# Kernel optimization log

Measured on AMD Instinct MI355X. Metric: run time of the kernel, lower is better.

## Reference

```python
import jax, jax.numpy as jnp
import numpy as np

B, N, E, D, H, HW, L = 16, 32, 256, 256, 8, 784, 4
DH = D // H
FF = 4 * D
BN = B * N
BE = B * E
SCALE = 1.0 / np.sqrt(DH)


def _ln(x, g, b):
    m = x.mean(-1, keepdims=True)
    v = ((x - m) ** 2).mean(-1, keepdims=True)
    return (x - m) * jax.lax.rsqrt(v + 1e-5) * g + b


def setup_inputs() -> dict:
    key = jax.random.key(0)
    ks = iter(jax.random.split(key, 64))
    def w(shape, s=0.05):
        return jax.random.normal(next(ks), shape, jnp.float32) * s
    inp = {
        'nodes': w((B, N, D), 1.0),
        'edges': w((B, E, D), 1.0),
        'images': w((B, HW, D), 1.0),
        'mask': jnp.zeros((B * H, N + E, HW), jnp.float32),
        'node_enc': w((BN, D), 1.0),
        'edge_enc': w((BE, D), 1.0),
        'ln1_g': jnp.ones((L, D), jnp.float32), 'ln1_b': jnp.zeros((L, D), jnp.float32),
        'Wqkv': w((L, D, 3 * D)), 'bqkv': jnp.zeros((L, 3 * D), jnp.float32),
        'Wo': w((L, D, D)), 'bo': jnp.zeros((L, D), jnp.float32),
        'ls1': jnp.full((L, D), 0.1, jnp.float32),
        'ln2_g': jnp.ones((L, D), jnp.float32), 'ln2_b': jnp.zeros((L, D), jnp.float32),
        'Wn1': w((L, D, D)), 'bn1': jnp.zeros((L, D), jnp.float32),
        'Wn2': w((L, D, D)), 'bn2': jnp.zeros((L, D), jnp.float32),
        'We': w((L, D, D)), 'be': jnp.zeros((L, D), jnp.float32),
        'attn_p': w((L, H, DH), 1.0),
        'Weo': w((L, D, D)), 'beo': jnp.zeros((L, D), jnp.float32),
        'Wno': w((L, D, D)), 'bno': jnp.zeros((L, D), jnp.float32),
        'ls2': jnp.full((L, D), 0.1, jnp.float32),
        'ln3_g': jnp.ones((L, D), jnp.float32), 'ln3_b': jnp.zeros((L, D), jnp.float32),
        'W1': w((L, D, FF)), 'b1': jnp.zeros((L, FF), jnp.float32),
        'W2': w((L, FF, D)), 'b2': jnp.zeros((L, D), jnp.float32),
        'ls3': jnp.full((L, D), 0.1, jnp.float32),
        'edge_index': jax.random.randint(next(ks), (2, BE), 0, BN, jnp.int32),
    }
    return inp


def reference(nodes, edges, images, mask, node_enc, edge_enc,
              ln1_g, ln1_b, Wqkv, bqkv, Wo, bo, ls1,
              ln2_g, ln2_b, Wn1, bn1, Wn2, bn2, We, be, attn_p, Weo, beo, Wno, bno, ls2,
              ln3_g, ln3_b, W1, b1, W2, b2, ls3, edge_index):
    idx0, idx1 = edge_index[0], edge_index[1]
    ne = jnp.concatenate([nodes, edges], axis=1)  # [B, N+E, D]
    mask4 = mask.reshape(B, H, N + E, HW)
    for l in range(L):
        # cross-attention ne -> images
        ne1n = _ln(ne, ln1_g[l], ln1_b[l])
        q = (ne1n @ Wqkv[l, :, :D] + bqkv[l, :D]).reshape(B, N + E, H, DH)
        k = (images @ Wqkv[l, :, D:2 * D] + bqkv[l, D:2 * D]).reshape(B, HW, H, DH)
        v = (images @ Wqkv[l, :, 2 * D:] + bqkv[l, 2 * D:]).reshape(B, HW, H, DH)
        scores = jnp.einsum('bqhd,bkhd->bhqk', q, k) * SCALE + mask4
        attn = jax.nn.softmax(scores, axis=-1)
        ctx = jnp.einsum('bhqk,bkhd->bqhd', attn, v).reshape(B, N + E, D)
        ne1 = ne + ls1[l] * (ctx @ Wo[l] + bo[l])
        # modified GAT on flattened graph
        ne2n = _ln(ne1, ln2_g[l], ln2_b[l])
        nodes_f = ne2n[:, :N].reshape(BN, D) + node_enc
        edges_f = ne2n[:, N:].reshape(BE, D) + edge_enc
        fn = (nodes_f @ Wn1[l] + bn1[l])[idx0]
        sn = (nodes_f @ Wn2[l] + bn2[l])[idx0]  # NOTE: original code uses edge_index[0] here too
        ep = edges_f @ We[l] + be[l]
        hidden = jax.nn.gelu(fn + sn + ep, approximate=False)  # [BE, D]
        pres = (hidden.reshape(BE, H, DH) * attn_p[l]).sum(-1)  # [BE, H]
        mseg = jax.ops.segment_max(pres, idx0, num_segments=BN)
        expv = jnp.exp(pres - mseg[idx0])
        denom = jax.ops.segment_sum(expv, idx0, num_segments=BN)
        alpha = expv / denom[idx0]  # scatter_softmax over destination nodes
        new_edges = hidden @ Weo[l] + beo[l]
        vals = (nodes_f[idx1] + new_edges) @ Wno[l] + bno[l]
        vals = vals.reshape(BE, H, DH) * alpha[..., None]
        new_nodes = jax.ops.segment_sum(vals.reshape(BE, D), idx0, num_segments=BN)
        gat = jnp.concatenate([new_nodes.reshape(B, N, D), new_edges.reshape(B, E, D)], axis=1)
        ne2 = ne1 + ls2[l] * gat
        # FFN
        ne3n = _ln(ne2, ln3_g[l], ln3_b[l])
        ffn = jax.nn.gelu(ne3n @ W1[l] + b1[l], approximate=False) @ W2[l] + b2[l]
        ne = ne2 + ls3[l] * ffn
    return ne
```

## Files before the change

kernel.cpp:

```cpp
#include <hip/hip_runtime.h>
#include <math.h>

static constexpr int B_  = 16;
static constexpr int N_  = 32;
static constexpr int E_  = 256;
static constexpr int D_  = 256;
static constexpr int H_  = 8;
static constexpr int HW_ = 784;
static constexpr int L_  = 4;
static constexpr int DH_ = 32;
static constexpr int FF_ = 1024;
static constexpr int BN_ = 512;
static constexpr int BE_ = 4096;
static constexpr int NE_ = 288;
static constexpr int NC_ = 13;
static constexpr int NBLK_ = B_ * H_ * 9;
#define SCALE_ 0.17677669529663687f

static constexpr size_t LAYER_W = 1114112;
static constexpr size_t OFF_Q   = 0;
static constexpr size_t OFF_K   = 65536;
static constexpr size_t OFF_WO  = 196608;
static constexpr size_t OFF_WN1 = 262144;
static constexpr size_t OFF_WE  = 393216;
static constexpr size_t OFF_WEO = 458752;
static constexpr size_t OFF_WNO = 524288;
static constexpr size_t OFF_W1  = 589824;
static constexpr size_t OFF_W2  = 851968;

typedef __attribute__((ext_vector_type(8))) short bf16x8;
typedef __attribute__((ext_vector_type(4))) float f32x4;

typedef __attribute__((address_space(1))) const unsigned int gas_uint;
typedef __attribute__((address_space(3))) unsigned int las_uint;

__device__ __forceinline__ void gload16(const unsigned short* g, unsigned short* lds) {
    __builtin_amdgcn_global_load_lds((gas_uint*)g, (las_uint*)lds, 16, 0, 0);
}

__device__ __forceinline__ float gelu_f(float x) {
    return 0.5f * x * (1.0f + erff(x * 0.7071067811865476f));
}

__device__ __forceinline__ unsigned short f2bf(float x) {
    unsigned u = __float_as_uint(x);
    u += 0x7FFFu + ((u >> 16) & 1u);
    return (unsigned short)(u >> 16);
}
__device__ __forceinline__ unsigned pack2bf(float a, float b) {
    return (unsigned)f2bf(a) | ((unsigned)f2bf(b) << 16);
}
__device__ __forceinline__ float bf2f(unsigned short u) {
    return __uint_as_float(((unsigned)u) << 16);
}


__global__ void concat_kernel(const float* __restrict__ nodes, const float* __restrict__ edges,
                              float* __restrict__ ne) {
    int tid = blockIdx.x * 256 + threadIdx.x;
    int d = tid & 255;
    int row = tid >> 8;
    int b = row / NE_, pos = row % NE_;
    float v = (pos < N_) ? nodes[(size_t)(b * N_ + pos) * D_ + d]
                         : edges[(size_t)(b * E_ + (pos - N_)) * D_ + d];
    ne[tid] = v;
}

__global__ void imgcast_kernel(const float* __restrict__ img, unsigned short* __restrict__ out) {
    int tid = blockIdx.x * 256 + threadIdx.x;
    const float* p = img + (size_t)tid * 8;
    float4 a = *(const float4*)(p);
    float4 b = *(const float4*)(p + 4);
    uint4 o = make_uint4(pack2bf(a.x, a.y), pack2bf(a.z, a.w),
                         pack2bf(b.x, b.y), pack2bf(b.z, b.w));
    *(uint4*)&out[(size_t)tid * 8] = o;
}

__global__ __launch_bounds__(128) void premask_kernel(const float* __restrict__ mask,
                                                      unsigned short* __restrict__ pmask) {
    const int bid = blockIdx.x;
    const int c = bid % NC_;
    const int bq = bid / NC_;
    const int h = bq & 7;
    const int qt = (bq >> 3) % 9;
    const int b = (bq >> 3) / 9;
    const int q0 = qt * 32, c0 = c * 64;
    __shared__ float ts[32][68];
    const int t = threadIdx.x;
    const int row = t >> 2, cg = (t & 3) * 16;
    const float* mrow = mask + ((size_t)(b * H_ + h) * NE_ + q0 + row) * (size_t)HW_;
    #pragma unroll
    for (int i = 0; i < 4; ++i) {
        int col = c0 + cg + i * 4;
        float4 m4;
        if (col + 4 <= HW_) {
            m4 = *(const float4*)(mrow + col);
        } else {
            m4.x = (col + 0 < HW_) ? mrow[col + 0] : -1e30f;
            m4.y = (col + 1 < HW_) ? mrow[col + 1] : -1e30f;
            m4.z = (col + 2 < HW_) ? mrow[col + 2] : -1e30f;
            m4.w = (col + 3 < HW_) ? mrow[col + 3] : -1e30f;
        }
        *(float4*)&ts[row][cg + i * 4] = m4;
    }
    __syncthreads();
    const int w = t >> 6, lg = (t & 63) >> 4, lr = t & 15;
    const int r0 = w * 16 + lg * 4;
    unsigned u[8];
    #pragma unroll
    for (int rg = 0; rg < 4; ++rg) {
        u[rg * 2 + 0] = pack2bf(ts[r0 + rg][0 * 16 + lr], ts[r0 + rg][1 * 16 + lr]);
        u[rg * 2 + 1] = pack2bf(ts[r0 + rg][2 * 16 + lr], ts[r0 + rg][3 * 16 + lr]);
    }
    uint4* dst = (uint4*)(pmask + (size_t)bid * 2048 + t * 16);
    dst[0] = make_uint4(u[0], u[1], u[2], u[3]);
    dst[1] = make_uint4(u[4], u[5], u[6], u[7]);
}

__device__ __forceinline__ float ln_from_val(float v, int d,
                                             const float* __restrict__ g, const float* __restrict__ bta,
                                             float* sh1, float* sh2) {
    float s = v, s2 = v * v;
    #pragma unroll
    for (int o = 32; o >= 1; o >>= 1) { s += __shfl_down(s, o); s2 += __shfl_down(s2, o); }
    int lane = d & 63, w = d >> 6;
    if (lane == 0) { sh1[w] = s; sh2[w] = s2; }
    __syncthreads();
    if (d == 0) {
        float a = sh1[0] + sh1[1] + sh1[2] + sh1[3];
        float c = sh2[0] + sh2[1] + sh2[2] + sh2[3];
        sh1[0] = a; sh2[0] = c;
    }
    __syncthreads();
    float mean = sh1[0] * (1.0f / D_);
    float var  = sh2[0] * (1.0f / D_) - mean * mean;
    float rstd = rsqrtf(var + 1e-5f);
    return (v - mean) * rstd * g[d] + bta[d];
}

__global__ __launch_bounds__(256) void ln_kernel(const float* __restrict__ x,
                                                 unsigned short* __restrict__ y,
                                                 const float* __restrict__ g,
                                                 const float* __restrict__ bta) {
    __shared__ float sh1[4], sh2[4];
    const int row = blockIdx.x, d = threadIdx.x;
    float v = x[(size_t)row * D_ + d];
    y[(size_t)row * D_ + d] = f2bf(ln_from_val(v, d, g, bta, sh1, sh2));
}

__global__ __launch_bounds__(256) void ln2enc_kernel(const float* __restrict__ x,
                                                     const float* __restrict__ g,
                                                     const float* __restrict__ bta,
                                                     const float* __restrict__ node_enc,
                                                     const float* __restrict__ edge_enc,
                                                     unsigned short* __restrict__ nodes_f,
                                                     unsigned short* __restrict__ edges_f) {
    __shared__ float sh1[4], sh2[4];
    const int row = blockIdx.x, d = threadIdx.x;
    float v = x[(size_t)row * D_ + d];
    float val = ln_from_val(v, d, g, bta, sh1, sh2);
    int b = row / NE_, pos = row % NE_;
    if (pos < N_) {
        int rn = b * N_ + pos;
        nodes_f[(size_t)rn * D_ + d] = f2bf(val + node_enc[(size_t)rn * D_ + d]);
    } else {
        int re = b * E_ + (pos - N_);
        edges_f[(size_t)re * D_ + d] = f2bf(val + edge_enc[(size_t)re * D_ + d]);
    }
}

__global__ __launch_bounds__(256) void gatres_ln_kernel(
    float* __restrict__ ne, const float* __restrict__ new_nodes,
    const float* __restrict__ new_edges, const float* __restrict__ ls2l,
    const float* __restrict__ g, const float* __restrict__ bta,
    unsigned short* __restrict__ lnb) {
    __shared__ float sh1[4], sh2[4];
    const int row = blockIdx.x, d = threadIdx.x;
    int b = row / NE_, pos = row % NE_;
    float gv = (pos < N_) ? new_nodes[(size_t)(b * N_ + pos) * D_ + d]
                          : new_edges[(size_t)(b * E_ + (pos - N_)) * D_ + d];
    float v = ne[(size_t)row * D_ + d] + ls2l[d] * gv;
    ne[(size_t)row * D_ + d] = v;
    lnb[(size_t)row * D_ + d] = f2bf(ln_from_val(v, d, g, bta, sh1, sh2));
}

__global__ __launch_bounds__(256) void wtrans_kernel(
    const float* __restrict__ Wqkv, const float* __restrict__ Wo,
    const float* __restrict__ Wn1,  const float* __restrict__ Wn2,
    const float* __restrict__ We,   const float* __restrict__ Weo,
    const float* __restrict__ Wno,  const float* __restrict__ W1,
    const float* __restrict__ W2,   unsigned short* __restrict__ wT)
{
    const int bid = blockIdx.x;
    const int l = bid / 1088;
    int tl = bid % 1088;
    const float* src; int ld, K, Nn; unsigned short* dst;
    if (tl < 576) {
        int mid = tl >> 6; tl &= 63;
        K = 256; Nn = 256;
        if (mid < 3) {
            src = Wqkv + (size_t)l * 256 * 768 + mid * 256; ld = 768;
            dst = wT + (size_t)l * LAYER_W + (size_t)mid * 65536;
        } else {
            const float* bases[6] = {Wo, Wn1, Wn2, We, Weo, Wno};
            src = bases[mid - 3] + (size_t)l * 65536; ld = 256;
            dst = wT + (size_t)l * LAYER_W + OFF_WO + (size_t)(mid - 3) * 65536;
        }
    } else if (tl < 832) {
        tl -= 576; K = 256; Nn = 1024;
        src = W1 + (size_t)l * 262144; ld = 1024;
        dst = wT + (size_t)l * LAYER_W + OFF_W1;
    } else {
        tl -= 832; K = 1024; Nn = 256;
        src = W2 + (size_t)l * 262144; ld = 256;
        dst = wT + (size_t)l * LAYER_W + OFF_W2;
    }
    const int ntn = Nn >> 5;
    const int k0 = (tl / ntn) << 5, n0 = (tl % ntn) << 5;
    __shared__ float ts[32][33];
    const int t = threadIdx.x;
    const int kl = t >> 5, nl = t & 31;
    #pragma unroll
    for (int rr = 0; rr < 4; ++rr)
        ts[kl + rr * 8][nl] = src[(size_t)(k0 + kl + rr * 8) * ld + n0 + nl];
    __syncthreads();
    const int onl = t >> 3, okl = (t & 7) << 2;
    ushort4 o;
    o.x = f2bf(ts[okl + 0][onl]); o.y = f2bf(ts[okl + 1][onl]);
    o.z = f2bf(ts[okl + 2][onl]); o.w = f2bf(ts[okl + 3][onl]);
    *(ushort4*)&dst[(size_t)(n0 + onl) * K + k0 + okl] = o;
}

template<int MODE, int OUTBF>
__global__ __launch_bounds__(256) void mgemm_kernel(
    const unsigned short* __restrict__ A, int lda,
    const unsigned short* __restrict__ Bt,
    const float* __restrict__ bias,
    const float* __restrict__ bias2,
    const float* __restrict__ res,
    const float* __restrict__ ls,
    void* __restrict__ Cv, int ldc, int K)
{
    __shared__ __align__(16) unsigned short As[64 * 64];
    __shared__ __align__(16) unsigned short Bs[64 * 64];
    const int m0 = blockIdx.y * 64, n0 = blockIdx.x * 64;
    const int t = threadIdx.x;
    const int l = t & 63, w = t >> 6;
    const int wr = (w >> 1) * 32, wc = (w & 1) * 32;
    const int frow = l & 15, kg = l >> 4;
    const int srow = w * 8 + (l >> 3);
    const int scolh = 8 * ((l & 7) ^ (l >> 3));
    const int ldsoff = w * 512;
    const int sw = (frow & 7) << 3;
    f32x4 acc[2][2];
    acc[0][0] = (f32x4){0.f,0.f,0.f,0.f}; acc[0][1] = acc[0][0];
    acc[1][0] = acc[0][0];                acc[1][1] = acc[0][0];
    for (int k0 = 0; k0 < K; k0 += 64) {
        const unsigned short* ga = A  + (size_t)(m0 + srow) * lda + k0 + scolh;
        const unsigned short* gb = Bt + (size_t)(n0 + srow) * K   + k0 + scolh;
        gload16(ga,                As + ldsoff);
        gload16(ga + 32 * lda,     As + ldsoff + 2048);
        gload16(gb,                Bs + ldsoff);
        gload16(gb + (size_t)32 * K, Bs + ldsoff + 2048);
        __syncthreads();
        #pragma unroll
        for (int kk = 0; kk < 2; ++kk) {
            const int off = (kk * 32 + kg * 8) ^ sw;
            bf16x8 af0 = *(const bf16x8*)&As[(wr + frow) * 64 + off];
            bf16x8 af1 = *(const bf16x8*)&As[(wr + 16 + frow) * 64 + off];
            bf16x8 bf0 = *(const bf16x8*)&Bs[(wc + frow) * 64 + off];
            bf16x8 bf1 = *(const bf16x8*)&Bs[(wc + 16 + frow) * 64 + off];
            acc[0][0] = __builtin_amdgcn_mfma_f32_16x16x32_bf16(af0, bf0, acc[0][0], 0, 0, 0);
            acc[0][1] = __builtin_amdgcn_mfma_f32_16x16x32_bf16(af0, bf1, acc[0][1], 0, 0, 0);
            acc[1][0] = __builtin_amdgcn_mfma_f32_16x16x32_bf16(af1, bf0, acc[1][0], 0, 0, 0);
            acc[1][1] = __builtin_amdgcn_mfma_f32_16x16x32_bf16(af1, bf1, acc[1][1], 0, 0, 0);
        }
        __syncthreads();
    }
    #pragma unroll
    for (int fr = 0; fr < 2; ++fr) {
        #pragma unroll
        for (int fc = 0; fc < 2; ++fc) {
            int n = n0 + wc + fc * 16 + frow;
            float bv = (bias2 != nullptr && n >= 256) ? bias2[n - 256] : bias[n];
            float lv = (MODE == 2) ? ls[n] : 0.f;
            #pragma unroll
            for (int rg = 0; rg < 4; ++rg) {
                int m = m0 + wr + fr * 16 + kg * 4 + rg;
                float vv = acc[fr][fc][rg] + bv;
                if (MODE == 1) vv = gelu_f(vv);
                if (MODE == 2) vv = res[(size_t)m * ldc + n] + lv * vv;
                if (OUTBF) ((unsigned short*)Cv)[(size_t)m * ldc + n] = f2bf(vv);
                else       ((float*)Cv)[(size_t)m * ldc + n] = vv;
            }
        }
    }
}

__global__ __launch_bounds__(128) void attn_kernel(
    const unsigned short* __restrict__ q, const unsigned short* __restrict__ kv,
    const unsigned short* __restrict__ pmask, unsigned short* __restrict__ ctx)
{
    const int bid = blockIdx.x;
    const int h = bid & 7;
    const int qt = (bid >> 3) % 9;
    const int b = (bid >> 3) / 9;
    const int q0 = qt * 32;
    const int t = threadIdx.x;
    const int w = t >> 6, l = t & 63;
    const int lr = l & 15, lg = l >> 4;

    __shared__ unsigned short Ks[2][64][40];
    __shared__ unsigned short Vs[2][32][72];
    __shared__ unsigned short Pl[2][16][72];

    bf16x8 qfrag = *(const bf16x8*)(q + ((size_t)(b * NE_ + q0 + w * 16 + lr)) * D_ + h * DH_ + lg * 8);

    const int kkey = t >> 1, kdh = (t & 1) * 16;
    const int vdh = (t & 7) * 4, vk0 = (t >> 3) * 2;
    const unsigned short* kbase = kv + ((size_t)b * HW_) * 512 + h * DH_;
    const unsigned short* vbase = kv + ((size_t)b * HW_) * 512 + 256 + h * DH_;
    const uint4* mbase = (const uint4*)(pmask + (size_t)bid * NC_ * 2048 + t * 16);

    uint4 kq0, kq1;
    ushort4 va[2], vb4[2];
    uint4 mc0, mc1, mn0, mn1;

    auto issue_kv = [&](int c0) {
        {
            int key = c0 + kkey;
            bool ok = key < HW_;
            const unsigned short* kp = kbase + (size_t)(ok ? key : 0) * 512 + kdh;
            kq0 = *(const uint4*)(kp);
            kq1 = *(const uint4*)(kp + 8);
            if (!ok) { kq0 = make_uint4(0,0,0,0); kq1 = kq0; }
        }
        #pragma unroll
        for (int r = 0; r < 2; ++r) {
            int key = c0 + vk0 + 32 * r;
            bool ok0 = key < HW_, ok1 = (key + 1) < HW_;
            const unsigned short* vp = vbase + (size_t)(ok0 ? key : 0) * 512 + vdh;
            va[r]  = *(const ushort4*)(vp);
            vb4[r] = *(const ushort4*)(vp + (ok1 ? 512 : 0));
            if (!ok0) va[r]  = make_ushort4(0,0,0,0);
            if (!ok1) vb4[r] = make_ushort4(0,0,0,0);
        }
    };
    auto write_kv = [&](int bufi) {
        *(uint4*)&Ks[bufi][kkey][kdh]     = kq0;
        *(uint4*)&Ks[bufi][kkey][kdh + 8] = kq1;
        #pragma unroll
        for (int r = 0; r < 2; ++r) {
            const unsigned short* a = (const unsigned short*)&va[r];
            const unsigned short* c = (const unsigned short*)&vb4[r];
            #pragma unroll
            for (int i = 0; i < 4; ++i)
                *(unsigned*)&Vs[bufi][vdh + i][vk0 + 32 * r] = (unsigned)a[i] | ((unsigned)c[i] << 16);
        }
    };

    f32x4 oacc[2];
    oacc[0] = (f32x4){0.f, 0.f, 0.f, 0.f}; oacc[1] = oacc[0];
    float m_i[4] = {-INFINITY, -INFINITY, -INFINITY, -INFINITY};
    float l_i[4] = {0.f, 0.f, 0.f, 0.f};

    issue_kv(0);
    mc0 = mbase[0]; mc1 = mbase[1];
    write_kv(0);
    mn0 = mbase[128]; mn1 = mbase[129];
    __syncthreads();

    for (int c = 0; c < NC_; ++c) {
        const int c0 = c * 64;
        const int cb = c & 1, nb = cb ^ 1;
        if (c + 1 < NC_) issue_kv(c0 + 64);

        f32x4 sacc[4];
        #pragma unroll
        for (int fc = 0; fc < 4; ++fc) {
            sacc[fc] = (f32x4){0.f, 0.f, 0.f, 0.f};
            bf16x8 kf = *(const bf16x8*)&Ks[cb][fc * 16 + lr][lg * 8];
            sacc[fc] = __builtin_amdgcn_mfma_f32_16x16x32_bf16(qfrag, kf, sacc[fc], 0, 0, 0);
        }
        float s[4][4];
        {
            unsigned uw[8] = {mc0.x, mc0.y, mc0.z, mc0.w, mc1.x, mc1.y, mc1.z, mc1.w};
            #pragma unroll
            for (int rg = 0; rg < 4; ++rg) {
                s[0][rg] = sacc[0][rg] * SCALE_ + bf2f((unsigned short)(uw[rg * 2] & 0xffff));
                s[1][rg] = sacc[1][rg] * SCALE_ + bf2f((unsigned short)(uw[rg * 2] >> 16));
                s[2][rg] = sacc[2][rg] * SCALE_ + bf2f((unsigned short)(uw[rg * 2 + 1] & 0xffff));
                s[3][rg] = sacc[3][rg] * SCALE_ + bf2f((unsigned short)(uw[rg * 2 + 1] >> 16));
            }
        }

        float mloc[4];
        #pragma unroll
        for (int rg = 0; rg < 4; ++rg)
            mloc[rg] = fmaxf(fmaxf(s[0][rg], s[1][rg]), fmaxf(s[2][rg], s[3][rg]));
        #pragma unroll
        for (int off = 1; off < 16; off <<= 1)
            #pragma unroll
            for (int rg = 0; rg < 4; ++rg)
                mloc[rg] = fmaxf(mloc[rg], __shfl_xor(mloc[rg], off));
        float scl[4], lloc[4];
        #pragma unroll
        for (int rg = 0; rg < 4; ++rg) {
            float mn = fmaxf(m_i[rg], mloc[rg]);
            scl[rg] = __expf(m_i[rg] - mn);
            m_i[rg] = mn;
        }
        #pragma unroll
        for (int rg = 0; rg < 4; ++rg) {
            float acc = 0.f;
            #pragma unroll
            for (int fc = 0; fc < 4; ++fc) {
                float p = __expf(s[fc][rg] - m_i[rg]);
                s[fc][rg] = p;
                acc += p;
            }
            lloc[rg] = acc;
        }
        #pragma unroll
        for (int off = 1; off < 16; off <<= 1)
            #pragma unroll
            for (int rg = 0; rg < 4; ++rg)
                lloc[rg] += __shfl_xor(lloc[rg], off);
        #pragma unroll
        for (int rg = 0; rg < 4; ++rg) {
            l_i[rg] = l_i[rg] * scl[rg] + lloc[rg];
            oacc[0][rg] *= scl[rg];
            oacc[1][rg] *= scl[rg];
        }

        #pragma unroll
        for (int fc = 0; fc < 4; ++fc)
            #pragma unroll
            for (int rg = 0; rg < 4; ++rg)
                Pl[w][lg * 4 + rg][fc * 16 + lr] = f2bf(s[fc][rg]);
        #pragma unroll
        for (int ks2 = 0; ks2 < 2; ++ks2) {
            bf16x8 pf = *(const bf16x8*)&Pl[w][lr][ks2 * 32 + lg * 8];
            #pragma unroll
            for (int d2 = 0; d2 < 2; ++d2) {
                bf16x8 vf = *(const bf16x8*)&Vs[cb][d2 * 16 + lr][ks2 * 32 + lg * 8];
                oacc[d2] = __builtin_amdgcn_mfma_f32_16x16x32_bf16(pf, vf, oacc[d2], 0, 0, 0);
            }
        }

        mc0 = mn0; mc1 = mn1;
        if (c + 2 < NC_) {
            mn0 = mbase[(c + 2) * 128];
            mn1 = mbase[(c + 2) * 128 + 1];
        }
        if (c + 1 < NC_) {
            write_kv(nb);
            __syncthreads();
        }
    }

    unsigned short* cbase = ctx + ((size_t)(b * NE_ + q0 + w * 16 + lg * 4)) * D_ + h * DH_;
    #pragma unroll
    for (int rg = 0; rg < 4; ++rg) {
        float inv = 1.0f / l_i[rg];
        #pragma unroll
        for (int d2 = 0; d2 < 2; ++d2)
            cbase[(size_t)rg * D_ + d2 * 16 + lr] = f2bf(oacc[d2][rg] * inv);
    }
}


__global__ __launch_bounds__(256) void hidden_kernel(
    const float* __restrict__ gn12,
    unsigned short* __restrict__ hid, const int* __restrict__ idx0,
    const float* __restrict__ attn_p_l, float* __restrict__ pres) {
    int e = blockIdx.x;
    int d = threadIdx.x;
    int n = idx0[e];
    float x = bf2f(hid[(size_t)e * D_ + d]) + gn12[(size_t)n * 512 + d] + gn12[(size_t)n * 512 + 256 + d];
    float hv = gelu_f(x);
    hid[(size_t)e * D_ + d] = f2bf(hv);
    float pr = hv * attn_p_l[d];
    #pragma unroll
    for (int o = 1; o < 32; o <<= 1) pr += __shfl_xor(pr, o);
    if ((d & 31) == 0) pres[e * H_ + (d >> 5)] = pr;
}

__global__ void segsoft_kernel(const float* __restrict__ pres, const int* __restrict__ csr_off,
                               const int* __restrict__ csr_perm,
                               float* __restrict__ mseg, float* __restrict__ denom) {
    int tid = blockIdx.x * 256 + threadIdx.x;
    int n = tid >> 3, h = tid & 7;
    int s = csr_off[n], e2 = csr_off[n + 1];
    float mx = -INFINITY;
    for (int i = s; i < e2; ++i) mx = fmaxf(mx, pres[csr_perm[i] * H_ + h]);
    float sum = 0.f;
    for (int i = s; i < e2; ++i) sum += expf(pres[csr_perm[i] * H_ + h] - mx);
    mseg[tid] = mx;
    denom[tid] = sum;
}

__global__ void vin_kernel(const unsigned short* __restrict__ nodes_f,
                           const float* __restrict__ new_edges,
                           const int* __restrict__ idx1, unsigned short* __restrict__ vin) {
    int tid = blockIdx.x * 256 + threadIdx.x;
    int e = tid >> 8, d = tid & 255;
    vin[tid] = f2bf(bf2f(nodes_f[(size_t)idx1[e] * D_ + d]) + new_edges[tid]);
}

__global__ __launch_bounds__(256) void nodeagg_kernel(
    const float* __restrict__ vals, const float* __restrict__ pres,
    const float* __restrict__ mseg, const float* __restrict__ denom,
    const int* __restrict__ csr_off, const int* __restrict__ csr_perm,
    float* __restrict__ new_nodes) {
    int n = blockIdx.x;
    int d = threadIdx.x;
    int s = csr_off[n], e2 = csr_off[n + 1];
    int h = d >> 5;
    float ms = mseg[n * H_ + h];
    float rd = 1.0f / denom[n * H_ + h];
    float acc = 0.f;
    for (int i = s; i < e2; ++i) {
        int e = csr_perm[i];
        float a = expf(pres[e * H_ + h] - ms) * rd;
        acc += vals[(size_t)e * D_ + d] * a;
    }
    new_nodes[(size_t)n * D_ + d] = acc;
}


__global__ void zero_counts(int* counts) {
    int t = blockIdx.x * 256 + threadIdx.x;
    if (t < BN_) counts[t] = 0;
}

__global__ void csr_count(const int* __restrict__ idx0, int* __restrict__ counts) {
    int e = blockIdx.x * 256 + threadIdx.x;
    if (e < BE_) atomicAdd(&counts[idx0[e]], 1);
}

__global__ __launch_bounds__(512) void csr_scan(const int* __restrict__ counts, int* __restrict__ csr_off) {
    __shared__ int buf[BN_];
    int t = threadIdx.x;
    int c = counts[t];
    buf[t] = c;
    __syncthreads();
    for (int o = 1; o < BN_; o <<= 1) {
        int add = (t >= o) ? buf[t - o] : 0;
        __syncthreads();
        buf[t] += add;
        __syncthreads();
    }
    csr_off[t] = buf[t] - c;
    if (t == BN_ - 1) csr_off[BN_] = buf[t];
}

__global__ __launch_bounds__(64) void csr_fill(const int* __restrict__ idx0,
                                               const int* __restrict__ csr_off,
                                               int* __restrict__ csr_perm) {
    int n = blockIdx.x;
    int lane = threadIdx.x;
    int w = csr_off[n];
    for (int c0 = 0; c0 < BE_; c0 += 64) {
        int e = c0 + lane;
        bool m = (idx0[e] == n);
        unsigned long long bal = __ballot(m);
        if (m) {
            int pre = __popcll(bal & ((1ull << lane) - 1ull));
            csr_perm[w + pre] = e;
        }
        w += __popcll(bal);
    }
}


static void launch_mgemm(hipStream_t s, int mode, int outbf,
                         const unsigned short* A, int lda, const unsigned short* Bt,
                         const float* bias, const float* bias2, const float* res, const float* ls,
                         void* C, int ldc, int M, int N, int K) {
    dim3 g(N / 64, M / 64);
    if (mode == 0) {
        if (outbf) mgemm_kernel<0,1><<<g, 256, 0, s>>>(A, lda, Bt, bias, bias2, res, ls, C, ldc, K);
        else       mgemm_kernel<0,0><<<g, 256, 0, s>>>(A, lda, Bt, bias, bias2, res, ls, C, ldc, K);
    } else if (mode == 1) {
        mgemm_kernel<1,1><<<g, 256, 0, s>>>(A, lda, Bt, bias, bias2, res, ls, C, ldc, K);
    } else {
        mgemm_kernel<2,0><<<g, 256, 0, s>>>(A, lda, Bt, bias, bias2, res, ls, C, ldc, K);
    }
}

extern "C" void kernel_launch(void* const* d_in, const int* in_sizes, int n_in,
                              void* d_out, int out_size, void* d_ws, size_t ws_size,
                              hipStream_t stream) {
    const float* nodes    = (const float*)d_in[0];
    const float* edges    = (const float*)d_in[1];
    const float* images   = (const float*)d_in[2];
    const float* mask     = (const float*)d_in[3];
    const float* node_enc = (const float*)d_in[4];
    const float* edge_enc = (const float*)d_in[5];
    const float* ln1_g = (const float*)d_in[6];
    const float* ln1_b = (const float*)d_in[7];
    const float* Wqkv  = (const float*)d_in[8];
    const float* bqkv  = (const float*)d_in[9];
    const float* Wo    = (const float*)d_in[10];
    const float* bo    = (const float*)d_in[11];
    const float* ls1   = (const float*)d_in[12];
    const float* ln2_g = (const float*)d_in[13];
    const float* ln2_b = (const float*)d_in[14];
    const float* Wn1   = (const float*)d_in[15];
    const float* bn1   = (const float*)d_in[16];
    const float* Wn2   = (const float*)d_in[17];
    const float* bn2   = (const float*)d_in[18];
    const float* We    = (const float*)d_in[19];
    const float* be    = (const float*)d_in[20];
    const float* attn_p= (const float*)d_in[21];
    const float* Weo   = (const float*)d_in[22];
    const float* beo   = (const float*)d_in[23];
    const float* Wno   = (const float*)d_in[24];
    const float* bno   = (const float*)d_in[25];
    const float* ls2   = (const float*)d_in[26];
    const float* ln3_g = (const float*)d_in[27];
    const float* ln3_b = (const float*)d_in[28];
    const float* W1    = (const float*)d_in[29];
    const float* b1    = (const float*)d_in[30];
    const float* W2    = (const float*)d_in[31];
    const float* b2    = (const float*)d_in[32];
    const float* ls3   = (const float*)d_in[33];
    const int*   edge_index = (const int*)d_in[34];
    const int* idx0 = edge_index;
    const int* idx1 = edge_index + BE_;

    float* ne = (float*)d_out;

    float* cur = (float*)d_ws;
    auto alloc = [&](size_t nfl) { float* p = cur; cur += nfl; return p; };
    auto allocbf = [&](size_t nbf) { float* p = cur; cur += (nbf + 1) / 2; return (unsigned short*)p; };

    unsigned short* lnbuf   = allocbf((size_t)B_ * NE_ * D_);
    unsigned short* qb      = allocbf((size_t)B_ * NE_ * D_);
    unsigned short* kvb     = allocbf((size_t)B_ * HW_ * 512);
    unsigned short* ffnh    = kvb;
    unsigned short* imgbf   = allocbf((size_t)B_ * HW_ * D_);
    unsigned short* ctxb    = allocbf((size_t)B_ * NE_ * D_);
    unsigned short* nodes_f = allocbf((size_t)BN_ * D_);
    unsigned short* edges_f = allocbf((size_t)BE_ * D_);
    unsigned short* hid     = allocbf((size_t)BE_ * D_);
    unsigned short* vin     = allocbf((size_t)BE_ * D_);
    unsigned short* pmaskb  = allocbf((size_t)NBLK_ * NC_ * 2048);
    float* gn12     = alloc((size_t)BN_ * 512);
    float* pres     = alloc((size_t)BE_ * H_);
    float* mseg     = alloc((size_t)BN_ * H_);
    float* denom    = alloc((size_t)BN_ * H_);
    float* new_edges= alloc((size_t)BE_ * D_);
    float* valsb    = alloc((size_t)BE_ * D_);
    float* new_nodes= alloc((size_t)BN_ * D_);
    int* counts   = (int*)cur; cur += BN_;
    int* csr_off  = (int*)cur; cur += BN_ + 4;
    int* csr_perm = (int*)cur; cur += BE_;
    cur = (float*)(((uintptr_t)cur + 255) & ~(uintptr_t)255);
    unsigned short* wT = (unsigned short*)cur;

    wtrans_kernel<<<4 * 1088, 256, 0, stream>>>(Wqkv, Wo, Wn1, Wn2, We, Weo, Wno, W1, W2, wT);
    imgcast_kernel<<<(B_ * HW_ * D_) / (256 * 8), 256, 0, stream>>>(images, imgbf);
    premask_kernel<<<NBLK_ * NC_, 128, 0, stream>>>(mask, pmaskb);
    zero_counts<<<2, 256, 0, stream>>>(counts);
    csr_count<<<BE_ / 256, 256, 0, stream>>>(idx0, counts);
    csr_scan<<<1, 512, 0, stream>>>(counts, csr_off);
    csr_fill<<<BN_, 64, 0, stream>>>(idx0, csr_off, csr_perm);
    concat_kernel<<<(B_ * NE_ * D_) / 256, 256, 0, stream>>>(nodes, edges, ne);

    for (int l = 0; l < L_; ++l) {
        const unsigned short* wTl = wT + (size_t)l * LAYER_W;
        const float* bqkv_l = bqkv + (size_t)l * 3 * D_;

        ln_kernel<<<B_ * NE_, 256, 0, stream>>>(ne, lnbuf, ln1_g + l * D_, ln1_b + l * D_);
        launch_mgemm(stream, 0, 1, lnbuf, D_, wTl + OFF_Q, bqkv_l, nullptr, nullptr, nullptr,
                     qb, D_, B_ * NE_, D_, D_);
        launch_mgemm(stream, 0, 1, imgbf, D_, wTl + OFF_K, bqkv_l + D_, nullptr, nullptr, nullptr,
                     kvb, 512, B_ * HW_, 512, D_);
        attn_kernel<<<NBLK_, 128, 0, stream>>>(qb, kvb, pmaskb, ctxb);
        launch_mgemm(stream, 2, 0, ctxb, D_, wTl + OFF_WO, bo + l * D_, nullptr, ne, ls1 + l * D_,
                     ne, D_, B_ * NE_, D_, D_);

        ln2enc_kernel<<<B_ * NE_, 256, 0, stream>>>(ne, ln2_g + l * D_, ln2_b + l * D_,
                                                    node_enc, edge_enc, nodes_f, edges_f);
        launch_mgemm(stream, 0, 0, nodes_f, D_, wTl + OFF_WN1, bn1 + l * D_, bn2 + l * D_,
                     nullptr, nullptr, gn12, 512, BN_, 512, D_);
        launch_mgemm(stream, 0, 1, edges_f, D_, wTl + OFF_WE, be + l * D_, nullptr, nullptr, nullptr,
                     hid, D_, BE_, D_, D_);
        hidden_kernel<<<BE_, 256, 0, stream>>>(gn12, hid, idx0, attn_p + (size_t)l * H_ * DH_, pres);
        segsoft_kernel<<<(BN_ * H_) / 256, 256, 0, stream>>>(pres, csr_off, csr_perm, mseg, denom);
        launch_mgemm(stream, 0, 0, hid, D_, wTl + OFF_WEO, beo + l * D_, nullptr, nullptr, nullptr,
                     new_edges, D_, BE_, D_, D_);
        vin_kernel<<<(BE_ * D_) / 256, 256, 0, stream>>>(nodes_f, new_edges, idx1, vin);
        launch_mgemm(stream, 0, 0, vin, D_, wTl + OFF_WNO, bno + l * D_, nullptr, nullptr, nullptr,
                     valsb, D_, BE_, D_, D_);
        nodeagg_kernel<<<BN_, 256, 0, stream>>>(valsb, pres, mseg, denom, csr_off, csr_perm, new_nodes);
        gatres_ln_kernel<<<B_ * NE_, 256, 0, stream>>>(ne, new_nodes, new_edges, ls2 + l * D_,
                                                       ln3_g + l * D_, ln3_b + l * D_, lnbuf);

        launch_mgemm(stream, 1, 1, lnbuf, D_, wTl + OFF_W1, b1 + l * FF_, nullptr, nullptr, nullptr,
                     ffnh, FF_, B_ * NE_, FF_, D_);
        launch_mgemm(stream, 2, 0, ffnh, FF_, wTl + OFF_W2, b2 + l * D_, nullptr, ne, ls3 + l * D_,
                     ne, D_, B_ * NE_, D_, FF_);
    }
}
```

Before: 720.5 us.

## Skip mask preprocessing when mask is all-zero and batch paired GEMM launches

Adds a kernel that scans the mask for any nonzero bits and sets a device flag. When the flag is clear, premask exits early and attention skips the mask loads, keeping only tail padding for out-of-range keys. Separately, the Q and KV projections, and the node and edge projections, are merged into one grouped GEMM launch each to cut launch count and fill the GPU better. The mask check still reads the full mask every call, but it is a runtime check rather than an assumption about the inputs.

New measurement: 619.6 us. 1.16x faster.

```diff
diff --git a/kernel.cpp b/kernel.cpp
--- a/kernel.cpp
+++ b/kernel.cpp
@@ -76,8 +76,30 @@
     *(uint4*)&out[(size_t)tid * 8] = o;
 }
 
+__global__ void zeroinit_kernel(int* counts, int* maskflag) {
+    int t = blockIdx.x * 256 + threadIdx.x;
+    if (t < BN_) counts[t] = 0;
+    if (t == 0) *maskflag = 0;
+}
+
+__global__ __launch_bounds__(256) void maskchk_kernel(const float* __restrict__ mask,
+                                                      int* __restrict__ flag) {
+    const size_t total = (size_t)B_ * H_ * NE_ * HW_ / 4;
+    const uint4* m = (const uint4*)mask;
+    unsigned acc = 0;
+    for (size_t i = (size_t)blockIdx.x * 256 + threadIdx.x; i < total; i += (size_t)gridDim.x * 256) {
+        uint4 v = m[i];
+        acc |= v.x | v.y | v.z | v.w;
+    }
+    unsigned long long bal = __ballot(acc != 0);
+    if (bal != 0 && (threadIdx.x & 63) == (__ffsll((long long)bal) - 1))
+        atomicOr(flag, 1);
+}
+
 __global__ __launch_bounds__(128) void premask_kernel(const float* __restrict__ mask,
-                                                      unsigned short* __restrict__ pmask) {
+                                                      unsigned short* __restrict__ pmask,
+                                                      const int* __restrict__ flag) {
+    if (*flag == 0) return;
     const int bid = blockIdx.x;
     const int c = bid % NC_;
     const int bq = bid / NC_;
@@ -230,6 +252,16 @@
     o.z = f2bf(ts[okl + 2][onl]); o.w = f2bf(ts[okl + 3][onl]);
     *(ushort4*)&dst[(size_t)(n0 + onl) * K + k0 + okl] = o;
 }
+
+
+struct GArgs {
+    const unsigned short* A;
+    const unsigned short* Bt;
+    const float* bias;
+    const float* bias2;
+    void* C;
+    int lda, ldc, K, outbf, nbx;
+};
 
 template<int MODE, int OUTBF>
 __global__ __launch_bounds__(256) void mgemm_kernel(
@@ -297,9 +329,67 @@
     }
 }
 
+__global__ __launch_bounds__(256) void mgemm2_kernel(GArgs g0, GArgs g1, int nblk0) {
+    const bool first = (int)blockIdx.x < nblk0;
+    GArgs g = first ? g0 : g1;
+    const int bid = first ? blockIdx.x : blockIdx.x - nblk0;
+    __shared__ __align__(16) unsigned short As[64 * 64];
+    __shared__ __align__(16) unsigned short Bs[64 * 64];
+    const int m0 = (bid / g.nbx) * 64, n0 = (bid % g.nbx) * 64;
+    const int t = threadIdx.x;
+    const int l = t & 63, w = t >> 6;
+    const int wr = (w >> 1) * 32, wc = (w & 1) * 32;
+    const int frow = l & 15, kg = l >> 4;
+    const int srow = w * 8 + (l >> 3);
+    const int scolh = 8 * ((l & 7) ^ (l >> 3));
+    const int ldsoff = w * 512;
+    const int sw = (frow & 7) << 3;
+    f32x4 acc[2][2];
+    acc[0][0] = (f32x4){0.f,0.f,0.f,0.f}; acc[0][1] = acc[0][0];
+    acc[1][0] = acc[0][0];                acc[1][1] = acc[0][0];
+    for (int k0 = 0; k0 < g.K; k0 += 64) {
+        const unsigned short* ga = g.A  + (size_t)(m0 + srow) * g.lda + k0 + scolh;
+        const unsigned short* gb = g.Bt + (size_t)(n0 + srow) * g.K   + k0 + scolh;
+        gload16(ga,                  As + ldsoff);
+        gload16(ga + 32 * g.lda,     As + ldsoff + 2048);
+        gload16(gb,                  Bs + ldsoff);
+        gload16(gb + (size_t)32 * g.K, Bs + ldsoff + 2048);
+        __syncthreads();
+        #pragma unroll
+        for (int kk = 0; kk < 2; ++kk) {
+            const int off = (kk * 32 + kg * 8) ^ sw;
+            bf16x8 af0 = *(const bf16x8*)&As[(wr + frow) * 64 + off];
+            bf16x8 af1 = *(const bf16x8*)&As[(wr + 16 + frow) * 64 + off];
+            bf16x8 bf0 = *(const bf16x8*)&Bs[(wc + frow) * 64 + off];
+            bf16x8 bf1 = *(const bf16x8*)&Bs[(wc + 16 + frow) * 64 + off];
+            acc[0][0] = __builtin_amdgcn_mfma_f32_16x16x32_bf16(af0, bf0, acc[0][0], 0, 0, 0);
+            acc[0][1] = __builtin_amdgcn_mfma_f32_16x16x32_bf16(af0, bf1, acc[0][1], 0, 0, 0);
+            acc[1][0] = __builtin_amdgcn_mfma_f32_16x16x32_bf16(af1, bf0, acc[1][0], 0, 0, 0);
+            acc[1][1] = __builtin_amdgcn_mfma_f32_16x16x32_bf16(af1, bf1, acc[1][1], 0, 0, 0);
+        }
+        __syncthreads();
+    }
+    #pragma unroll
+    for (int fr = 0; fr < 2; ++fr) {
+        #pragma unroll
+        for (int fc = 0; fc < 2; ++fc) {
+            int n = n0 + wc + fc * 16 + frow;
+            float bv = (g.bias2 != nullptr && n >= 256) ? g.bias2[n - 256] : g.bias[n];
+            #pragma unroll
+            for (int rg = 0; rg < 4; ++rg) {
+                int m = m0 + wr + fr * 16 + kg * 4 + rg;
+                float vv = acc[fr][fc][rg] + bv;
+                if (g.outbf) ((unsigned short*)g.C)[(size_t)m * g.ldc + n] = f2bf(vv);
+                else         ((float*)g.C)[(size_t)m * g.ldc + n] = vv;
+            }
+        }
+    }
+}
+
 __global__ __launch_bounds__(128) void attn_kernel(
     const unsigned short* __restrict__ q, const unsigned short* __restrict__ kv,
-    const unsigned short* __restrict__ pmask, unsigned short* __restrict__ ctx)
+    const unsigned short* __restrict__ pmask, const int* __restrict__ maskflag,
+    unsigned short* __restrict__ ctx)
 {
     const int bid = blockIdx.x;
     const int h = bid & 7;
@@ -309,6 +399,7 @@
     const int t = threadIdx.x;
     const int w = t >> 6, l = t & 63;
     const int lr = l & 15, lg = l >> 4;
+    const int hasmask = *maskflag;
 
     __shared__ unsigned short Ks[2][64][40];
     __shared__ unsigned short Vs[2][32][72];
@@ -324,7 +415,7 @@
 
     uint4 kq0, kq1;
     ushort4 va[2], vb4[2];
-    uint4 mc0, mc1, mn0, mn1;
+    uint4 mc0 = make_uint4(0,0,0,0), mc1 = mc0, mn0 = mc0, mn1 = mc0;
 
     auto issue_kv = [&](int c0) {
         {
@@ -365,9 +456,9 @@
     float l_i[4] = {0.f, 0.f, 0.f, 0.f};
 
     issue_kv(0);
-    mc0 = mbase[0]; mc1 = mbase[1];
+    if (hasmask) { mc0 = mbase[0]; mc1 = mbase[1]; }
     write_kv(0);
-    mn0 = mbase[128]; mn1 = mbase[129];
+    if (hasmask) { mn0 = mbase[128]; mn1 = mbase[129]; }
     __syncthreads();
 
     for (int c = 0; c < NC_; ++c) {
@@ -383,7 +474,7 @@
             sacc[fc] = __builtin_amdgcn_mfma_f32_16x16x32_bf16(qfrag, kf, sacc[fc], 0, 0, 0);
         }
         float s[4][4];
-        {
+        if (hasmask) {
             unsigned uw[8] = {mc0.x, mc0.y, mc0.z, mc0.w, mc1.x, mc1.y, mc1.z, mc1.w};
             #pragma unroll
             for (int rg = 0; rg < 4; ++rg) {
@@ -392,6 +483,15 @@
                 s[2][rg] = sacc[2][rg] * SCALE_ + bf2f((unsigned short)(uw[rg * 2 + 1] & 0xffff));
                 s[3][rg] = sacc[3][rg] * SCALE_ + bf2f((unsigned short)(uw[rg * 2 + 1] >> 16));
             }
+        } else {
+            const bool tailc = (c == NC_ - 1);
+            #pragma unroll
+            for (int fc = 0; fc < 4; ++fc) {
+                float pad = (tailc && (c0 + fc * 16 + lr) >= HW_) ? -1e30f : 0.f;
+                #pragma unroll
+                for (int rg = 0; rg < 4; ++rg)
+                    s[fc][rg] = sacc[fc][rg] * SCALE_ + pad;
+            }
         }
 
         float mloc[4];
@@ -448,10 +548,12 @@
             }
         }
 
-        mc0 = mn0; mc1 = mn1;
-        if (c + 2 < NC_) {
-            mn0 = mbase[(c + 2) * 128];
-            mn1 = mbase[(c + 2) * 128 + 1];
+        if (hasmask) {
+            mc0 = mn0; mc1 = mn1;
+            if (c + 2 < NC_) {
+                mn0 = mbase[(c + 2) * 128];
+                mn1 = mbase[(c + 2) * 128 + 1];
+            }
         }
         if (c + 1 < NC_) {
             write_kv(nb);
@@ -528,11 +630,6 @@
     new_nodes[(size_t)n * D_ + d] = acc;
 }
 
-
-__global__ void zero_counts(int* counts) {
-    int t = blockIdx.x * 256 + threadIdx.x;
-    if (t < BN_) counts[t] = 0;
-}
 
 __global__ void csr_count(const int* __restrict__ idx0, int* __restrict__ counts) {
     int e = blockIdx.x * 256 + threadIdx.x;
@@ -657,13 +754,15 @@
     int* counts   = (int*)cur; cur += BN_;
     int* csr_off  = (int*)cur; cur += BN_ + 4;
     int* csr_perm = (int*)cur; cur += BE_;
+    int* maskflag = (int*)cur; cur += 4;
     cur = (float*)(((uintptr_t)cur + 255) & ~(uintptr_t)255);
     unsigned short* wT = (unsigned short*)cur;
 
+    zeroinit_kernel<<<2, 256, 0, stream>>>(counts, maskflag);
+    maskchk_kernel<<<2048, 256, 0, stream>>>(mask, maskflag);
     wtrans_kernel<<<4 * 1088, 256, 0, stream>>>(Wqkv, Wo, Wn1, Wn2, We, Weo, Wno, W1, W2, wT);
     imgcast_kernel<<<(B_ * HW_ * D_) / (256 * 8), 256, 0, stream>>>(images, imgbf);
-    premask_kernel<<<NBLK_ * NC_, 128, 0, stream>>>(mask, pmaskb);
-    zero_counts<<<2, 256, 0, stream>>>(counts);
+    premask_kernel<<<NBLK_ * NC_, 128, 0, stream>>>(mask, pmaskb, maskflag);
     csr_count<<<BE_ / 256, 256, 0, stream>>>(idx0, counts);
     csr_scan<<<1, 512, 0, stream>>>(counts, csr_off);
     csr_fill<<<BN_, 64, 0, stream>>>(idx0, csr_off, csr_perm);
@@ -674,20 +773,26 @@
         const float* bqkv_l = bqkv + (size_t)l * 3 * D_;
 
         ln_kernel<<<B_ * NE_, 256, 0, stream>>>(ne, lnbuf, ln1_g + l * D_, ln1_b + l * D_);
-        launch_mgemm(stream, 0, 1, lnbuf, D_, wTl + OFF_Q, bqkv_l, nullptr, nullptr, nullptr,
-                     qb, D_, B_ * NE_, D_, D_);
-        launch_mgemm(stream, 0, 1, imgbf, D_, wTl + OFF_K, bqkv_l + D_, nullptr, nullptr, nullptr,
-                     kvb, 512, B_ * HW_, 512, D_);
-        attn_kernel<<<NBLK_, 128, 0, stream>>>(qb, kvb, pmaskb, ctxb);
+        {
+            GArgs gq { lnbuf, wTl + OFF_Q, bqkv_l, nullptr, qb, 256, 256, 256, 1, 4 };
+            GArgs gkv{ imgbf, wTl + OFF_K, bqkv_l + D_, nullptr, kvb, 256, 512, 256, 1, 8 };
+            int nb0 = (B_ * NE_ / 64) * 4;
+            int nb1 = (B_ * HW_ / 64) * 8;
+            mgemm2_kernel<<<nb0 + nb1, 256, 0, stream>>>(gq, gkv, nb0);
+        }
+        attn_kernel<<<NBLK_, 128, 0, stream>>>(qb, kvb, pmaskb, maskflag, ctxb);
         launch_mgemm(stream, 2, 0, ctxb, D_, wTl + OFF_WO, bo + l * D_, nullptr, ne, ls1 + l * D_,
                      ne, D_, B_ * NE_, D_, D_);
 
         ln2enc_kernel<<<B_ * NE_, 256, 0, stream>>>(ne, ln2_g + l * D_, ln2_b + l * D_,
                                                     node_enc, edge_enc, nodes_f, edges_f);
-        launch_mgemm(stream, 0, 0, nodes_f, D_, wTl + OFF_WN1, bn1 + l * D_, bn2 + l * D_,
-                     nullptr, nullptr, gn12, 512, BN_, 512, D_);
-        launch_mgemm(stream, 0, 1, edges_f, D_, wTl + OFF_WE, be + l * D_, nullptr, nullptr, nullptr,
-                     hid, D_, BE_, D_, D_);
+        {
+            GArgs gn { nodes_f, wTl + OFF_WN1, bn1 + l * D_, bn2 + l * D_, gn12, 256, 512, 256, 0, 8 };
+            GArgs ge { edges_f, wTl + OFF_WE,  be + l * D_,  nullptr,      hid,  256, 256, 256, 1, 4 };
+            int nb0 = (BN_ / 64) * 8;
+            int nb1 = (BE_ / 64) * 4;
+            mgemm2_kernel<<<nb0 + nb1, 256, 0, stream>>>(gn, ge, nb0);
+        }
         hidden_kernel<<<BE_, 256, 0, stream>>>(gn12, hid, idx0, attn_p + (size_t)l * H_ * DH_, pres);
         segsoft_kernel<<<(BN_ * H_) / 256, 256, 0, stream>>>(pres, csr_off, csr_perm, mseg, denom);
         launch_mgemm(stream, 0, 0, hid, D_, wTl + OFF_WEO, beo + l * D_, nullptr, nullptr, nullptr,
```
